# Performance work log

Hardware: AMD Instinct MI355X
Metric: run time of the kernel (lower is better)

## Reference

```python
import jax, jax.numpy as jnp
import numpy as np

EPS = 1e-6
B, H, V, DH = 4096, 16, 8, 128


def setup_inputs() -> dict:
    key = jax.random.key(0)
    ks = jax.random.split(key, 7)
    s = 1.0 / np.sqrt(DH)  # ~ torch Linear init scale
    return {
        "iso_heads": jax.random.normal(ks[0], (B, H, DH), jnp.float32),
        "view_head_tokens": jax.random.normal(ks[1], (B, H, V, DH), jnp.float32),
        "pi": jax.random.uniform(ks[2], (B, H, V), jnp.float32),
        "Wq": jax.random.normal(ks[3], (H, DH, DH), jnp.float32) * s,
        "Wk": jax.random.normal(ks[4], (H, DH, DH), jnp.float32) * s,
        "Wv": jax.random.normal(ks[5], (H, DH, DH), jnp.float32) * s,
        "Wo": jax.random.normal(ks[6], (H, DH, DH), jnp.float32) * s,
    }


def reference(iso_heads, view_head_tokens, pi, Wq, Wk, Wv, Wo):
    # Per-head linears: torch Linear(y = x @ W.T), W stored (out, in) -> 'hed' (e=out, d=in)
    q = jnp.einsum("bhd,hed->bhe", iso_heads, Wq)            # [B,H,Dh]
    k = jnp.einsum("bhvd,hed->bhve", view_head_tokens, Wk)   # [B,H,V,Dh]
    v = jnp.einsum("bhvd,hed->bhve", view_head_tokens, Wv)   # [B,H,V,Dh]
    # Single-query attention per head with additive log-prior bias
    scores = jnp.einsum("bhd,bhvd->bhv", q, k) / jnp.sqrt(jnp.float32(DH))
    scores = scores + jnp.log(pi + EPS)
    attn = jax.nn.softmax(scores, axis=-1)                   # dropout = identity (eval)
    ctx = jnp.einsum("bhv,bhvd->bhd", attn, v)               # [B,H,Dh]
    out = jnp.einsum("bhd,hed->bhe", ctx, Wo)                # [B,H,Dh]
    return (out, attn)
```

## Files before the change

### kernel.cpp

```cpp
#include <hip/hip_runtime.h>
#include <cstdint>
#include <cstddef>

#define H_  16
#define V_  8
#define DH_ 128
#define B_  4096
#define BT  32
#define LDST 132

__global__ __launch_bounds__(256) void precompute_MN(
    const float* __restrict__ Wq, const float* __restrict__ Wk,
    const float* __restrict__ Wv, const float* __restrict__ Wo,
    float* __restrict__ Mmat, float* __restrict__ NTmat)
{
    const int bx    = blockIdx.x;
    const int which = bx & 1;
    const int h     = (bx >> 1) & 15;
    const int chunk = bx >> 5;
    const int tid   = threadIdx.x;
    const int col   = tid & 127;
    const int r0    = chunk * 16 + (tid >> 7) * 8;

    float acc[8];
#pragma unroll
    for (int r = 0; r < 8; ++r) acc[r] = 0.f;

    if (which == 0) {
        const float* wq = Wq + h * DH_ * DH_;
        const float* wk = Wk + h * DH_ * DH_;
        for (int e = 0; e < DH_; ++e) {
            const float bk = wk[e * DH_ + col];
#pragma unroll
            for (int r = 0; r < 8; ++r) acc[r] += wq[e * DH_ + r0 + r] * bk;
        }
        float* dst = Mmat + h * DH_ * DH_;
#pragma unroll
        for (int r = 0; r < 8; ++r) dst[(r0 + r) * DH_ + col] = acc[r];
    } else {
        const float* wo = Wo + h * DH_ * DH_;
        const float* wv = Wv + h * DH_ * DH_;
        for (int d = 0; d < DH_; ++d) {
            const float bv = wv[d * DH_ + col];
#pragma unroll
            for (int r = 0; r < 8; ++r) acc[r] += wo[(r0 + r) * DH_ + d] * bv;
        }
        float* dst = NTmat + h * DH_ * DH_;
#pragma unroll
        for (int r = 0; r < 8; ++r) dst[(size_t)col * DH_ + (r0 + r)] = acc[r];
    }
}

__global__ __launch_bounds__(256) void fused_attn(
    const float* __restrict__ iso, const float* __restrict__ view,
    const float* __restrict__ pi,
    const float* __restrict__ Mmat, const float* __restrict__ NTmat,
    float* __restrict__ out, float* __restrict__ attn_out)
{
    __shared__ float buf_s[BT][LDST];
    __shared__ float qk_s[BT][LDST];
    __shared__ float sc_s[BT][V_];
    __shared__ float attn_s[BT][V_];

    const int tid = threadIdx.x;
    const int h   = blockIdx.x >> 7;
    const int b0  = (blockIdx.x & 127) * BT;

#pragma unroll
    for (int i = 0; i < 4; ++i) {
        const int idx = tid + i * 256;
        const int b   = idx >> 5;
        const int dq  = idx & 31;
        const float4 v4 = *(const float4*)(iso + ((size_t)(b0 + b) * H_ + h) * DH_ + dq * 4);
        *(float4*)&buf_s[b][dq * 4] = v4;
    }
    __syncthreads();

    const int tx = tid & 31;
    const int ty = tid >> 5;

    {
        const float* Mh = Mmat + h * DH_ * DH_ + tx * 4;
        float acc[4][4];
#pragma unroll
        for (int i = 0; i < 4; ++i)
#pragma unroll
            for (int j = 0; j < 4; ++j) acc[i][j] = 0.f;

        for (int d = 0; d < DH_; d += 4) {
            const float4 m0 = *(const float4*)(Mh + (size_t)(d + 0) * DH_);
            const float4 m1 = *(const float4*)(Mh + (size_t)(d + 1) * DH_);
            const float4 m2 = *(const float4*)(Mh + (size_t)(d + 2) * DH_);
            const float4 m3 = *(const float4*)(Mh + (size_t)(d + 3) * DH_);
#pragma unroll
            for (int i = 0; i < 4; ++i) {
                const float4 a = *(const float4*)&buf_s[ty * 4 + i][d];
                acc[i][0] += a.x * m0.x + a.y * m1.x + a.z * m2.x + a.w * m3.x;
                acc[i][1] += a.x * m0.y + a.y * m1.y + a.z * m2.y + a.w * m3.y;
                acc[i][2] += a.x * m0.z + a.y * m1.z + a.z * m2.z + a.w * m3.z;
                acc[i][3] += a.x * m0.w + a.y * m1.w + a.z * m2.w + a.w * m3.w;
            }
        }
#pragma unroll
        for (int i = 0; i < 4; ++i)
            *(float4*)&qk_s[ty * 4 + i][tx * 4] =
                make_float4(acc[i][0], acc[i][1], acc[i][2], acc[i][3]);
    }
    __syncthreads();

    {
        const int wv   = tid >> 6;
        const int lane = tid & 63;
        const int half = lane >> 5;
        const int l32  = lane & 31;
#pragma unroll 4
        for (int it = 0; it < 32; ++it) {
            const int p  = wv * 64 + it * 2 + half;
            const int bl = p >> 3;
            const int v  = p & 7;
            const float4 w = *(const float4*)(view +
                (((size_t)(b0 + bl) * H_ + h) * V_ + v) * DH_ + l32 * 4);
            const float4 q = *(const float4*)&qk_s[bl][l32 * 4];
            float s = w.x * q.x + w.y * q.y + w.z * q.z + w.w * q.w;
            s += __shfl_xor(s, 1);
            s += __shfl_xor(s, 2);
            s += __shfl_xor(s, 4);
            s += __shfl_xor(s, 8);
            s += __shfl_xor(s, 16);
            if (l32 == 0) sc_s[bl][v] = s;
        }
    }
    __syncthreads();

    {
        const int bl = tid >> 3;
        const int v  = tid & 7;
        float sc = sc_s[bl][v] * 0.08838834764831845f;
        sc += logf(pi[((size_t)(b0 + bl) * H_ + h) * V_ + v] + 1e-6f);

        float mx = sc;
        mx = fmaxf(mx, __shfl_xor(mx, 1));
        mx = fmaxf(mx, __shfl_xor(mx, 2));
        mx = fmaxf(mx, __shfl_xor(mx, 4));
        const float ex = expf(sc - mx);
        float sm = ex;
        sm += __shfl_xor(sm, 1);
        sm += __shfl_xor(sm, 2);
        sm += __shfl_xor(sm, 4);
        const float at = ex / sm;
        attn_s[bl][v] = at;
        attn_out[((size_t)(b0 + bl) * H_ + h) * V_ + v] = at;
    }
    __syncthreads();

    {
        const int bg  = tid >> 5;
        const int l32 = tid & 31;
#pragma unroll
        for (int r = 0; r < 4; ++r) {
            const int b = r * 8 + bg;
            const float* vbase = view + (((size_t)(b0 + b) * H_ + h) * V_) * DH_ + l32 * 4;
            float4 c = make_float4(0.f, 0.f, 0.f, 0.f);
#pragma unroll
            for (int vv = 0; vv < V_; ++vv) {
                const float a = attn_s[b][vv];
                const float4 x = *(const float4*)(vbase + (size_t)vv * DH_);
                c.x += a * x.x; c.y += a * x.y; c.z += a * x.z; c.w += a * x.w;
            }
            *(float4*)&buf_s[b][l32 * 4] = c;
        }
    }
    __syncthreads();

    {
        const float* Nh = NTmat + h * DH_ * DH_ + tx * 4;
        float acc[4][4];
#pragma unroll
        for (int i = 0; i < 4; ++i)
#pragma unroll
            for (int j = 0; j < 4; ++j) acc[i][j] = 0.f;

        for (int dp = 0; dp < DH_; dp += 4) {
            const float4 n0 = *(const float4*)(Nh + (size_t)(dp + 0) * DH_);
            const float4 n1 = *(const float4*)(Nh + (size_t)(dp + 1) * DH_);
            const float4 n2 = *(const float4*)(Nh + (size_t)(dp + 2) * DH_);
            const float4 n3 = *(const float4*)(Nh + (size_t)(dp + 3) * DH_);
#pragma unroll
            for (int i = 0; i < 4; ++i) {
                const float4 a = *(const float4*)&buf_s[ty * 4 + i][dp];
                acc[i][0] += a.x * n0.x + a.y * n1.x + a.z * n2.x + a.w * n3.x;
                acc[i][1] += a.x * n0.y + a.y * n1.y + a.z * n2.y + a.w * n3.y;
                acc[i][2] += a.x * n0.z + a.y * n1.z + a.z * n2.z + a.w * n3.z;
                acc[i][3] += a.x * n0.w + a.y * n1.w + a.z * n2.w + a.w * n3.w;
            }
        }
#pragma unroll
        for (int i = 0; i < 4; ++i)
            *(float4*)(out + ((size_t)(b0 + ty * 4 + i) * H_ + h) * DH_ + tx * 4) =
                make_float4(acc[i][0], acc[i][1], acc[i][2], acc[i][3]);
    }
}

extern "C" void kernel_launch(void* const* d_in, const int* in_sizes, int n_in,
                              void* d_out, int out_size, void* d_ws, size_t ws_size,
                              hipStream_t stream)
{
    const float* iso  = (const float*)d_in[0];
    const float* view = (const float*)d_in[1];
    const float* pi   = (const float*)d_in[2];
    const float* Wq   = (const float*)d_in[3];
    const float* Wk   = (const float*)d_in[4];
    const float* Wv   = (const float*)d_in[5];
    const float* Wo   = (const float*)d_in[6];

    float* out  = (float*)d_out;
    float* attn = out + (size_t)B_ * H_ * DH_;

    float* Mmat  = (float*)d_ws;
    float* NTmat = Mmat + (size_t)H_ * DH_ * DH_;

    hipLaunchKernelGGL(precompute_MN, dim3(256), dim3(256), 0, stream,
                       Wq, Wk, Wv, Wo, Mmat, NTmat);
    hipLaunchKernelGGL(fused_attn, dim3(H_ * (B_ / BT)), dim3(256), 0, stream,
                       iso, view, pi, Mmat, NTmat, out, attn);
}
```

Measured before the change: 519.1 us.

## Halve batch tile, shrink blocks, reuse shared buffer, and parallelize weight precompute

The fused attention kernel now handles 16 batch rows per block with 128 threads and launch bounds requesting 8 blocks per CU. It drops the separate qk shared buffer by writing the projected query back into the input buffer after a barrier. The weight-product precompute switches from 8 rows per thread to one row per thread over 2048 blocks to expose more parallelism. The intent is higher occupancy and more blocks in flight. The cost is twice as many blocks, each re-reading the 64KB M and N matrices, and an extra barrier.

```diff
diff --git a/kernel.cpp b/kernel.cpp
--- a/kernel.cpp
+++ b/kernel.cpp
@@ -6,7 +6,7 @@
 #define V_  8
 #define DH_ 128
 #define B_  4096
-#define BT  32
+#define BT  16
 #define LDST 132
 
 __global__ __launch_bounds__(256) void precompute_MN(
@@ -20,55 +20,43 @@
     const int chunk = bx >> 5;
     const int tid   = threadIdx.x;
     const int col   = tid & 127;
-    const int r0    = chunk * 16 + (tid >> 7) * 8;
-
-    float acc[8];
-#pragma unroll
-    for (int r = 0; r < 8; ++r) acc[r] = 0.f;
-
+    const int r     = chunk * 2 + (tid >> 7);
+
+    float acc = 0.f;
     if (which == 0) {
         const float* wq = Wq + h * DH_ * DH_;
         const float* wk = Wk + h * DH_ * DH_;
-        for (int e = 0; e < DH_; ++e) {
-            const float bk = wk[e * DH_ + col];
-#pragma unroll
-            for (int r = 0; r < 8; ++r) acc[r] += wq[e * DH_ + r0 + r] * bk;
-        }
-        float* dst = Mmat + h * DH_ * DH_;
-#pragma unroll
-        for (int r = 0; r < 8; ++r) dst[(r0 + r) * DH_ + col] = acc[r];
+#pragma unroll 8
+        for (int e = 0; e < DH_; ++e)
+            acc += wq[e * DH_ + r] * wk[e * DH_ + col];
+        Mmat[h * DH_ * DH_ + (size_t)r * DH_ + col] = acc;
     } else {
         const float* wo = Wo + h * DH_ * DH_;
         const float* wv = Wv + h * DH_ * DH_;
-        for (int d = 0; d < DH_; ++d) {
-            const float bv = wv[d * DH_ + col];
-#pragma unroll
-            for (int r = 0; r < 8; ++r) acc[r] += wo[(r0 + r) * DH_ + d] * bv;
-        }
-        float* dst = NTmat + h * DH_ * DH_;
-#pragma unroll
-        for (int r = 0; r < 8; ++r) dst[(size_t)col * DH_ + (r0 + r)] = acc[r];
+#pragma unroll 8
+        for (int d = 0; d < DH_; ++d)
+            acc += wo[(size_t)r * DH_ + d] * wv[d * DH_ + col];
+        NTmat[h * DH_ * DH_ + (size_t)col * DH_ + r] = acc;
     }
 }
 
-__global__ __launch_bounds__(256) void fused_attn(
+__global__ __launch_bounds__(128, 8) void fused_attn(
     const float* __restrict__ iso, const float* __restrict__ view,
     const float* __restrict__ pi,
     const float* __restrict__ Mmat, const float* __restrict__ NTmat,
     float* __restrict__ out, float* __restrict__ attn_out)
 {
     __shared__ float buf_s[BT][LDST];
-    __shared__ float qk_s[BT][LDST];
     __shared__ float sc_s[BT][V_];
-    __shared__ float attn_s[BT][V_];
+    __shared__ float at_s[BT][V_];
 
     const int tid = threadIdx.x;
-    const int h   = blockIdx.x >> 7;
-    const int b0  = (blockIdx.x & 127) * BT;
+    const int h   = blockIdx.x >> 8;
+    const int b0  = (blockIdx.x & 255) * BT;
 
 #pragma unroll
     for (int i = 0; i < 4; ++i) {
-        const int idx = tid + i * 256;
+        const int idx = tid + i * 128;
         const int b   = idx >> 5;
         const int dq  = idx & 31;
         const float4 v4 = *(const float4*)(iso + ((size_t)(b0 + b) * H_ + h) * DH_ + dq * 4);
@@ -79,9 +67,10 @@
     const int tx = tid & 31;
     const int ty = tid >> 5;
 
+    float acc[4][4];
+
     {
         const float* Mh = Mmat + h * DH_ * DH_ + tx * 4;
-        float acc[4][4];
 #pragma unroll
         for (int i = 0; i < 4; ++i)
 #pragma unroll
@@ -101,26 +90,28 @@
                 acc[i][3] += a.x * m0.w + a.y * m1.w + a.z * m2.w + a.w * m3.w;
             }
         }
-#pragma unroll
-        for (int i = 0; i < 4; ++i)
-            *(float4*)&qk_s[ty * 4 + i][tx * 4] =
-                make_float4(acc[i][0], acc[i][1], acc[i][2], acc[i][3]);
-    }
-    __syncthreads();
-
-    {
-        const int wv   = tid >> 6;
+    }
+    __syncthreads();
+
+#pragma unroll
+    for (int i = 0; i < 4; ++i)
+        *(float4*)&buf_s[ty * 4 + i][tx * 4] =
+            make_float4(acc[i][0], acc[i][1], acc[i][2], acc[i][3]);
+    __syncthreads();
+
+    {
+        const int wv_  = tid >> 6;
         const int lane = tid & 63;
         const int half = lane >> 5;
         const int l32  = lane & 31;
 #pragma unroll 4
         for (int it = 0; it < 32; ++it) {
-            const int p  = wv * 64 + it * 2 + half;
+            const int p  = wv_ * 64 + it * 2 + half;
             const int bl = p >> 3;
             const int v  = p & 7;
             const float4 w = *(const float4*)(view +
                 (((size_t)(b0 + bl) * H_ + h) * V_ + v) * DH_ + l32 * 4);
-            const float4 q = *(const float4*)&qk_s[bl][l32 * 4];
+            const float4 q = *(const float4*)&buf_s[bl][l32 * 4];
             float s = w.x * q.x + w.y * q.y + w.z * q.z + w.w * q.w;
             s += __shfl_xor(s, 1);
             s += __shfl_xor(s, 2);
@@ -148,7 +139,7 @@
         sm += __shfl_xor(sm, 2);
         sm += __shfl_xor(sm, 4);
         const float at = ex / sm;
-        attn_s[bl][v] = at;
+        at_s[bl][v] = at;
         attn_out[((size_t)(b0 + bl) * H_ + h) * V_ + v] = at;
     }
     __syncthreads();
@@ -158,12 +149,12 @@
         const int l32 = tid & 31;
 #pragma unroll
         for (int r = 0; r < 4; ++r) {
-            const int b = r * 8 + bg;
+            const int b = r * 4 + bg;
             const float* vbase = view + (((size_t)(b0 + b) * H_ + h) * V_) * DH_ + l32 * 4;
             float4 c = make_float4(0.f, 0.f, 0.f, 0.f);
 #pragma unroll
             for (int vv = 0; vv < V_; ++vv) {
-                const float a = attn_s[b][vv];
+                const float a = at_s[b][vv];
                 const float4 x = *(const float4*)(vbase + (size_t)vv * DH_);
                 c.x += a * x.x; c.y += a * x.y; c.z += a * x.z; c.w += a * x.w;
             }
@@ -174,7 +165,6 @@
 
     {
         const float* Nh = NTmat + h * DH_ * DH_ + tx * 4;
-        float acc[4][4];
 #pragma unroll
         for (int i = 0; i < 4; ++i)
 #pragma unroll
@@ -219,8 +209,8 @@
     float* Mmat  = (float*)d_ws;
     float* NTmat = Mmat + (size_t)H_ * DH_ * DH_;
 
-    hipLaunchKernelGGL(precompute_MN, dim3(256), dim3(256), 0, stream,
+    hipLaunchKernelGGL(precompute_MN, dim3(2048), dim3(256), 0, stream,
                        Wq, Wk, Wv, Wo, Mmat, NTmat);
-    hipLaunchKernelGGL(fused_attn, dim3(H_ * (B_ / BT)), dim3(256), 0, stream,
+    hipLaunchKernelGGL(fused_attn, dim3(H_ * (B_ / BT)), dim3(128), 0, stream,
                        iso, view, pi, Mmat, NTmat, out, attn);
 }
```

Result: faster. 506.9 us (-2.4%).
